# Kernel optimization log

Hardware: AMD Instinct MI355X
Metric: run time of the kernel (lower is better)

## Reference

```python
import jax, jax.numpy as jnp
import numpy as np

B, D, K, L, V = 4096, 512, 10, 256, 80


def setup_inputs() -> dict:
    key = jax.random.key(0)
    k1, k2, k3, k4, k5, k6 = jax.random.split(key, 6)
    inputs = jax.random.normal(k1, (B, D), dtype=jnp.float32)
    prev_kappa = jax.random.uniform(k2, (B, K), dtype=jnp.float32)
    char_ids = jax.random.randint(k3, (B, L), 0, V)
    char_seq_one_hot = jax.nn.one_hot(char_ids, V, dtype=jnp.float32)
    sequence_lengths = jax.random.randint(k4, (B,), 1, L + 1).astype(jnp.int32)
    # Dense params: VarianceScaling(scale=2.0, fan_avg) ~ N(0, 2/((D+3K)/2)) truncated
    std = np.sqrt(2.0 / ((D + 3 * K) / 2.0))
    W = (jax.random.truncated_normal(k5, -2.0, 2.0, (D, 3 * K)) * std).astype(jnp.float32)
    b = jnp.zeros((3 * K,), dtype=jnp.float32)
    kappa_scale = jnp.float32(-2.5)
    return {
        "inputs": inputs,
        "prev_kappa": prev_kappa,
        "char_seq_one_hot": char_seq_one_hot,
        "sequence_lengths": sequence_lengths,
        "W": W,
        "b": b,
        "kappa_scale": kappa_scale,
    }


def reference(inputs, prev_kappa, char_seq_one_hot, sequence_lengths, W, b, kappa_scale):
    raw = inputs @ W + b  # [B, 3K]
    alpha_hat, beta_hat, kappa_hat = jnp.split(raw, 3, axis=1)  # each [B, K]
    alpha = jnp.exp(jnp.clip(alpha_hat, -8.0, 8.0))
    beta = jnp.exp(jnp.clip(beta_hat, -8.0, 8.0))
    delta_kappa = jnp.exp(jnp.clip(kappa_hat + kappa_scale, -8.0, 5.0))
    kappa = prev_kappa + delta_kappa  # [B, K]

    char_len = char_seq_one_hot.shape[1]
    u = jnp.arange(1, char_len + 1, dtype=jnp.float32)  # [L]
    # exponent: [B, K, L]
    exponent = -beta[:, :, None] * jnp.square(kappa[:, :, None] - u[None, None, :])
    exponent = jnp.clip(exponent, -50.0, 0.0)
    phi = jnp.sum(alpha[:, :, None] * jnp.exp(exponent), axis=1)  # [B, L]

    seq_mask = (jnp.arange(char_len)[None, :] < sequence_lengths[:, None]).astype(jnp.float32)
    phi = phi * seq_mask
    phi = jnp.where(jnp.isfinite(phi), phi, 0.0)

    w = jnp.einsum("bl,blv->bv", phi, char_seq_one_hot)  # [B, V]
    w = jnp.where(jnp.isfinite(w), w, 0.0)
    return (w, kappa)
```

## Files before the change

### kernel.cpp

```cpp
#include <hip/hip_runtime.h>

#define B_ 4096
#define D_ 512
#define K_ 10
#define L_ 256
#define V_ 80

__global__ __launch_bounds__(256) void fused_kernel(
    const float* __restrict__ x,
    const float* __restrict__ prev_kappa,
    const float* __restrict__ oh,
    const int*   __restrict__ seqlen,
    const float* __restrict__ W,
    const float* __restrict__ bias,
    const float* __restrict__ kappa_scale,
    float* __restrict__ out_w,
    float* __restrict__ out_kappa)
{
    const int b    = blockIdx.x;
    const int tid  = threadIdx.x;
    const int wave = tid >> 6;
    const int lane = tid & 63;

    __shared__ float s_raw[32];
    __shared__ float s_a[K_], s_b[K_], s_k[K_];
    __shared__ float s_phi[L_];
    __shared__ float s_w[V_];

    const float* xr = x + (size_t)b * D_;
    const int jbase = wave * 8;
    const int jcnt  = (jbase < 24) ? 8 : 6;

    float acc[8];
#pragma unroll
    for (int jj = 0; jj < 8; ++jj) acc[jj] = 0.f;

#pragma unroll
    for (int i = 0; i < 8; ++i) {
        const int d = lane + 64 * i;
        const float xv = xr[d];
        const float* wrow = W + d * 30 + jbase;
#pragma unroll
        for (int jj = 0; jj < 8; ++jj) {
            if (jj < 6 || jbase < 24)
                acc[jj] = fmaf(xv, wrow[jj], acc[jj]);
        }
    }

#pragma unroll
    for (int jj = 0; jj < 8; ++jj) {
#pragma unroll
        for (int s = 32; s >= 1; s >>= 1)
            acc[jj] += __shfl_xor(acc[jj], s, 64);
    }

    if (lane < jcnt) {
        float v = acc[0];
#pragma unroll
        for (int jj = 1; jj < 8; ++jj) v = (lane == jj) ? acc[jj] : v;
        s_raw[jbase + lane] = v;
    }
    if (tid < V_) s_w[tid] = 0.f;
    __syncthreads();

    if (tid < K_) {
        const float a_hat = s_raw[tid]      + bias[tid];
        const float b_hat = s_raw[10 + tid] + bias[10 + tid];
        const float k_hat = s_raw[20 + tid] + bias[20 + tid];

        s_a[tid] = __expf(fminf(fmaxf(a_hat, -8.f), 8.f));
        s_b[tid] = __expf(fminf(fmaxf(b_hat, -8.f), 8.f));
        const float dk = __expf(fminf(fmaxf(k_hat + kappa_scale[0], -8.f), 5.f));
        const float kp = prev_kappa[b * K_ + tid] + dk;
        s_k[tid] = kp;
        out_kappa[b * K_ + tid] = kp;
    }
    const int sl = seqlen[b];
    __syncthreads();

    if (tid < sl) {
        const float u = (float)(tid + 1);
        float phi = 0.f;
#pragma unroll
        for (int k = 0; k < K_; ++k) {
            const float diff = s_k[k] - u;
            float e = -s_b[k] * diff * diff;
            e = fmaxf(e, -50.f);
            phi = fmaf(s_a[k], __expf(e), phi);
        }
        s_phi[tid] = phi;
    }
    __syncthreads();

    const int total4 = sl * (V_ / 4);
    const float4* ohb = (const float4*)(oh + (size_t)b * (L_ * V_));
    for (int f = tid; f < total4; f += 256) {
        const float4 vals = ohb[f];
        const int base = f * 4;
        const float vv[4] = {vals.x, vals.y, vals.z, vals.w};
#pragma unroll
        for (int c = 0; c < 4; ++c) {
            if (vv[c] != 0.f) {
                const int idx = base + c;
                const int l = idx / V_;
                const int v = idx - l * V_;
                atomicAdd(&s_w[v], s_phi[l] * vv[c]);
            }
        }
    }
    __syncthreads();

    if (tid < V_) out_w[b * V_ + tid] = s_w[tid];
}

extern "C" void kernel_launch(void* const* d_in, const int* in_sizes, int n_in,
                              void* d_out, int out_size, void* d_ws, size_t ws_size,
                              hipStream_t stream) {
    const float* x          = (const float*)d_in[0];
    const float* prev_kappa = (const float*)d_in[1];
    const float* oh         = (const float*)d_in[2];
    const int*   seqlen     = (const int*)d_in[3];
    const float* W          = (const float*)d_in[4];
    const float* bias       = (const float*)d_in[5];
    const float* kscale     = (const float*)d_in[6];

    float* out   = (float*)d_out;
    float* out_w = out;
    float* out_k = out + B_ * V_;

    fused_kernel<<<B_, 256, 0, stream>>>(x, prev_kappa, oh, seqlen, W, bias,
                                         kscale, out_w, out_k);
}
```

Baseline: 467.6 us.

## Split GEMV into separate 4-row-per-block kernel and unroll one-hot scatter

```diff
diff --git a/kernel.cpp b/kernel.cpp
--- a/kernel.cpp
+++ b/kernel.cpp
@@ -6,75 +6,106 @@
 #define L_ 256
 #define V_ 80
 
-__global__ __launch_bounds__(256) void fused_kernel(
+__global__ __launch_bounds__(256) void gemv_kernel(
     const float* __restrict__ x,
     const float* __restrict__ prev_kappa,
-    const float* __restrict__ oh,
-    const int*   __restrict__ seqlen,
     const float* __restrict__ W,
     const float* __restrict__ bias,
-    const float* __restrict__ kappa_scale,
-    float* __restrict__ out_w,
+    const float* __restrict__ kscale,
+    float* __restrict__ ws_alpha,
+    float* __restrict__ ws_beta,
     float* __restrict__ out_kappa)
 {
-    const int b    = blockIdx.x;
     const int tid  = threadIdx.x;
     const int wave = tid >> 6;
     const int lane = tid & 63;
+    const int r0   = blockIdx.x * 4;
+    const int jbase = wave * 8;
+    const int jcnt  = (wave == 3) ? 6 : 8;
 
-    __shared__ float s_raw[32];
+    const float* xb = x + (size_t)r0 * D_;
+
+    float acc[4][8];
+#pragma unroll
+    for (int r = 0; r < 4; ++r)
+#pragma unroll
+        for (int jj = 0; jj < 8; ++jj) acc[r][jj] = 0.f;
+
+#pragma unroll
+    for (int i = 0; i < 8; ++i) {
+        const int d = lane + 64 * i;
+        const float* wrow = W + d * 30 + jbase;
+        float wv[8];
+#pragma unroll
+        for (int jj = 0; jj < 8; ++jj)
+            wv[jj] = (jj < 6 || wave < 3) ? wrow[jj] : 0.f;
+#pragma unroll
+        for (int r = 0; r < 4; ++r) {
+            const float xv = xb[r * D_ + d];
+#pragma unroll
+            for (int jj = 0; jj < 8; ++jj)
+                acc[r][jj] = fmaf(xv, wv[jj], acc[r][jj]);
+        }
+    }
+
+#pragma unroll
+    for (int r = 0; r < 4; ++r)
+#pragma unroll
+        for (int jj = 0; jj < 8; ++jj)
+#pragma unroll
+            for (int s = 32; s >= 1; s >>= 1)
+                acc[r][jj] += __shfl_xor(acc[r][jj], s, 64);
+
+    __shared__ float s_raw[4][30];
+    if (lane < jcnt) {
+#pragma unroll
+        for (int r = 0; r < 4; ++r) {
+            float v = acc[r][0];
+#pragma unroll
+            for (int jj = 1; jj < 8; ++jj) v = (lane == jj) ? acc[r][jj] : v;
+            s_raw[r][jbase + lane] = v;
+        }
+    }
+    __syncthreads();
+
+    if (tid < 40) {
+        const int r = tid / 10;
+        const int k = tid - r * 10;
+        const int row = r0 + r;
+
+        const float a_hat = s_raw[r][k]      + bias[k];
+        const float b_hat = s_raw[r][10 + k] + bias[10 + k];
+        const float k_hat = s_raw[r][20 + k] + bias[20 + k];
+
+        ws_alpha[row * K_ + k] = __expf(fminf(fmaxf(a_hat, -8.f), 8.f));
+        ws_beta[row * K_ + k]  = __expf(fminf(fmaxf(b_hat, -8.f), 8.f));
+        const float dk = __expf(fminf(fmaxf(k_hat + kscale[0], -8.f), 5.f));
+        out_kappa[row * K_ + k] = prev_kappa[row * K_ + k] + dk;
+    }
+}
+
+__global__ __launch_bounds__(256) void scatter_kernel(
+    const float* __restrict__ oh,
+    const int*   __restrict__ seqlen,
+    const float* __restrict__ ws_alpha,
+    const float* __restrict__ ws_beta,
+    const float* __restrict__ kappa,
+    float* __restrict__ out_w)
+{
+    const int b   = blockIdx.x;
+    const int tid = threadIdx.x;
+
     __shared__ float s_a[K_], s_b[K_], s_k[K_];
     __shared__ float s_phi[L_];
     __shared__ float s_w[V_];
 
-    const float* xr = x + (size_t)b * D_;
-    const int jbase = wave * 8;
-    const int jcnt  = (jbase < 24) ? 8 : 6;
-
-    float acc[8];
-#pragma unroll
-    for (int jj = 0; jj < 8; ++jj) acc[jj] = 0.f;
-
-#pragma unroll
-    for (int i = 0; i < 8; ++i) {
-        const int d = lane + 64 * i;
-        const float xv = xr[d];
-        const float* wrow = W + d * 30 + jbase;
-#pragma unroll
-        for (int jj = 0; jj < 8; ++jj) {
-            if (jj < 6 || jbase < 24)
-                acc[jj] = fmaf(xv, wrow[jj], acc[jj]);
-        }
-    }
-
-#pragma unroll
-    for (int jj = 0; jj < 8; ++jj) {
-#pragma unroll
-        for (int s = 32; s >= 1; s >>= 1)
-            acc[jj] += __shfl_xor(acc[jj], s, 64);
-    }
-
-    if (lane < jcnt) {
-        float v = acc[0];
-#pragma unroll
-        for (int jj = 1; jj < 8; ++jj) v = (lane == jj) ? acc[jj] : v;
-        s_raw[jbase + lane] = v;
+    if (tid < K_) {
+        s_a[tid] = ws_alpha[b * K_ + tid];
+        s_b[tid] = ws_beta[b * K_ + tid];
+        s_k[tid] = kappa[b * K_ + tid];
     }
     if (tid < V_) s_w[tid] = 0.f;
-    __syncthreads();
 
-    if (tid < K_) {
-        const float a_hat = s_raw[tid]      + bias[tid];
-        const float b_hat = s_raw[10 + tid] + bias[10 + tid];
-        const float k_hat = s_raw[20 + tid] + bias[20 + tid];
-
-        s_a[tid] = __expf(fminf(fmaxf(a_hat, -8.f), 8.f));
-        s_b[tid] = __expf(fminf(fmaxf(b_hat, -8.f), 8.f));
-        const float dk = __expf(fminf(fmaxf(k_hat + kappa_scale[0], -8.f), 5.f));
-        const float kp = prev_kappa[b * K_ + tid] + dk;
-        s_k[tid] = kp;
-        out_kappa[b * K_ + tid] = kp;
-    }
     const int sl = seqlen[b];
     __syncthreads();
 
@@ -84,8 +115,7 @@
 #pragma unroll
         for (int k = 0; k < K_; ++k) {
             const float diff = s_k[k] - u;
-            float e = -s_b[k] * diff * diff;
-            e = fmaxf(e, -50.f);
+            float e = fmaxf(-s_b[k] * diff * diff, -50.f);
             phi = fmaf(s_a[k], __expf(e), phi);
         }
         s_phi[tid] = phi;
@@ -94,18 +124,31 @@
 
     const int total4 = sl * (V_ / 4);
     const float4* ohb = (const float4*)(oh + (size_t)b * (L_ * V_));
-    for (int f = tid; f < total4; f += 256) {
-        const float4 vals = ohb[f];
-        const int base = f * 4;
-        const float vv[4] = {vals.x, vals.y, vals.z, vals.w};
-#pragma unroll
-        for (int c = 0; c < 4; ++c) {
-            if (vv[c] != 0.f) {
-                const int idx = base + c;
-                const int l = idx / V_;
-                const int v = idx - l * V_;
-                atomicAdd(&s_w[v], s_phi[l] * vv[c]);
-            }
+
+    for (int f = tid; f < total4; f += 512) {
+        const float4 v0 = ohb[f];
+        const int f1 = f + 256;
+        const bool has1 = (f1 < total4);
+        float4 v1 = make_float4(0.f, 0.f, 0.f, 0.f);
+        if (has1) v1 = ohb[f1];
+
+        {
+            const int l  = f / 20;
+            const int vb = (f - l * 20) * 4;
+            const float p = s_phi[l];
+            if (v0.x != 0.f) atomicAdd(&s_w[vb + 0], p * v0.x);
+            if (v0.y != 0.f) atomicAdd(&s_w[vb + 1], p * v0.y);
+            if (v0.z != 0.f) atomicAdd(&s_w[vb + 2], p * v0.z);
+            if (v0.w != 0.f) atomicAdd(&s_w[vb + 3], p * v0.w);
+        }
+        if (has1) {
+            const int l  = f1 / 20;
+            const int vb = (f1 - l * 20) * 4;
+            const float p = s_phi[l];
+            if (v1.x != 0.f) atomicAdd(&s_w[vb + 0], p * v1.x);
+            if (v1.y != 0.f) atomicAdd(&s_w[vb + 1], p * v1.y);
+            if (v1.z != 0.f) atomicAdd(&s_w[vb + 2], p * v1.z);
+            if (v1.w != 0.f) atomicAdd(&s_w[vb + 3], p * v1.w);
         }
     }
     __syncthreads();
@@ -128,6 +171,12 @@
     float* out_w = out;
     float* out_k = out + B_ * V_;
 
-    fused_kernel<<<B_, 256, 0, stream>>>(x, prev_kappa, oh, seqlen, W, bias,
-                                         kscale, out_w, out_k);
+    float* wsf      = (float*)d_ws;
+    float* ws_alpha = wsf;
+    float* ws_beta  = wsf + B_ * K_;
+
+    gemv_kernel<<<B_ / 4, 256, 0, stream>>>(x, prev_kappa, W, bias, kscale,
+                                            ws_alpha, ws_beta, out_k);
+    scatter_kernel<<<B_, 256, 0, stream>>>(oh, seqlen, ws_alpha, ws_beta, out_k,
+                                           out_w);
 }
```

After: 434.9 us. 1.08x faster.

## Restructure projection GEMV via shared-memory x and per-column partial sums

Applied to the files above, without the earlier changes.

```diff
diff --git a/kernel.cpp b/kernel.cpp
--- a/kernel.cpp
+++ b/kernel.cpp
@@ -13,69 +13,61 @@
     const int*   __restrict__ seqlen,
     const float* __restrict__ W,
     const float* __restrict__ bias,
-    const float* __restrict__ kappa_scale,
+    const float* __restrict__ kscale,
     float* __restrict__ out_w,
     float* __restrict__ out_kappa)
 {
-    const int b    = blockIdx.x;
-    const int tid  = threadIdx.x;
-    const int wave = tid >> 6;
-    const int lane = tid & 63;
+    const int b   = blockIdx.x;
+    const int tid = threadIdx.x;
 
-    __shared__ float s_raw[32];
-    __shared__ float s_a[K_], s_b[K_], s_k[K_];
+    __shared__ float s_x[D_];
+    __shared__ float s_part[8][30];
+    __shared__ float s_abk[30];
     __shared__ float s_phi[L_];
     __shared__ float s_w[V_];
 
-    const float* xr = x + (size_t)b * D_;
-    const int jbase = wave * 8;
-    const int jcnt  = (jbase < 24) ? 8 : 6;
-
-    float acc[8];
-#pragma unroll
-    for (int jj = 0; jj < 8; ++jj) acc[jj] = 0.f;
-
-#pragma unroll
-    for (int i = 0; i < 8; ++i) {
-        const int d = lane + 64 * i;
-        const float xv = xr[d];
-        const float* wrow = W + d * 30 + jbase;
-#pragma unroll
-        for (int jj = 0; jj < 8; ++jj) {
-            if (jj < 6 || jbase < 24)
-                acc[jj] = fmaf(xv, wrow[jj], acc[jj]);
-        }
-    }
-
-#pragma unroll
-    for (int jj = 0; jj < 8; ++jj) {
-#pragma unroll
-        for (int s = 32; s >= 1; s >>= 1)
-            acc[jj] += __shfl_xor(acc[jj], s, 64);
-    }
-
-    if (lane < jcnt) {
-        float v = acc[0];
-#pragma unroll
-        for (int jj = 1; jj < 8; ++jj) v = (lane == jj) ? acc[jj] : v;
-        s_raw[jbase + lane] = v;
+    if (tid < 128) {
+        const float4* xg = (const float4*)(x + (size_t)b * D_);
+        ((float4*)s_x)[tid] = xg[tid];
     }
     if (tid < V_) s_w[tid] = 0.f;
     __syncthreads();
 
-    if (tid < K_) {
-        const float a_hat = s_raw[tid]      + bias[tid];
-        const float b_hat = s_raw[10 + tid] + bias[10 + tid];
-        const float k_hat = s_raw[20 + tid] + bias[20 + tid];
+    if (tid < 240) {
+        const int j = tid % 30;
+        const int g = tid / 30;
+        const float* xr = s_x + g * 64;
+        const float* wp = W + (size_t)(g * 64) * 30 + j;
 
-        s_a[tid] = __expf(fminf(fmaxf(a_hat, -8.f), 8.f));
-        s_b[tid] = __expf(fminf(fmaxf(b_hat, -8.f), 8.f));
-        const float dk = __expf(fminf(fmaxf(k_hat + kappa_scale[0], -8.f), 5.f));
-        const float kp = prev_kappa[b * K_ + tid] + dk;
-        s_k[tid] = kp;
-        out_kappa[b * K_ + tid] = kp;
+        float a0 = 0.f, a1 = 0.f, a2 = 0.f, a3 = 0.f;
+#pragma unroll 4
+        for (int i = 0; i < 64; i += 4) {
+            a0 = fmaf(xr[i + 0], wp[(i + 0) * 30], a0);
+            a1 = fmaf(xr[i + 1], wp[(i + 1) * 30], a1);
+            a2 = fmaf(xr[i + 2], wp[(i + 2) * 30], a2);
+            a3 = fmaf(xr[i + 3], wp[(i + 3) * 30], a3);
+        }
+        s_part[g][j] = (a0 + a1) + (a2 + a3);
     }
+    __syncthreads();
+
     const int sl = seqlen[b];
+
+    if (tid < 30) {
+        float v = bias[tid];
+#pragma unroll
+        for (int g = 0; g < 8; ++g) v += s_part[g][tid];
+
+        if (tid < 20) {
+            s_abk[tid] = __expf(fminf(fmaxf(v, -8.f), 8.f));
+        } else {
+            const int k = tid - 20;
+            const float dk = __expf(fminf(fmaxf(v + kscale[0], -8.f), 5.f));
+            const float kp = prev_kappa[b * K_ + k] + dk;
+            s_abk[tid] = kp;
+            out_kappa[b * K_ + k] = kp;
+        }
+    }
     __syncthreads();
 
     if (tid < sl) {
@@ -83,10 +75,9 @@
         float phi = 0.f;
 #pragma unroll
         for (int k = 0; k < K_; ++k) {
-            const float diff = s_k[k] - u;
-            float e = -s_b[k] * diff * diff;
-            e = fmaxf(e, -50.f);
-            phi = fmaf(s_a[k], __expf(e), phi);
+            const float diff = s_abk[20 + k] - u;
+            const float e = fmaxf(-s_abk[10 + k] * diff * diff, -50.f);
+            phi = fmaf(s_abk[k], __expf(e), phi);
         }
         s_phi[tid] = phi;
     }
@@ -96,17 +87,13 @@
     const float4* ohb = (const float4*)(oh + (size_t)b * (L_ * V_));
     for (int f = tid; f < total4; f += 256) {
         const float4 vals = ohb[f];
-        const int base = f * 4;
-        const float vv[4] = {vals.x, vals.y, vals.z, vals.w};
-#pragma unroll
-        for (int c = 0; c < 4; ++c) {
-            if (vv[c] != 0.f) {
-                const int idx = base + c;
-                const int l = idx / V_;
-                const int v = idx - l * V_;
-                atomicAdd(&s_w[v], s_phi[l] * vv[c]);
-            }
-        }
+        const int l  = f / 20;
+        const int vb = (f - l * 20) * 4;
+        const float p = s_phi[l];
+        if (vals.x != 0.f) atomicAdd(&s_w[vb + 0], p * vals.x);
+        if (vals.y != 0.f) atomicAdd(&s_w[vb + 1], p * vals.y);
+        if (vals.z != 0.f) atomicAdd(&s_w[vb + 2], p * vals.z);
+        if (vals.w != 0.f) atomicAdd(&s_w[vb + 3], p * vals.w);
     }
     __syncthreads();
 
```

After: 426.4 us. 8.8% less time.
